# Performance work log

Measured on AMD Instinct MI355X. Metric: run time of the kernel, lower is better.

Reference implementation:

```python
import jax, jax.numpy as jnp
import numpy as np

B, D, C = 8192, 1024, 4096  # batch, d_model, num_clusters (all active)
EPS = 1e-12  # matches F.normalize eps


def _l2_normalize(x):
    n = jnp.linalg.norm(x, axis=-1, keepdims=True)
    return x / jnp.maximum(n, EPS)


def setup_inputs() -> dict:
    key = jax.random.key(0)
    k1, k2 = jax.random.split(key)
    embedding = jax.random.normal(k1, (B, D), dtype=jnp.float32)
    centroids = jax.random.normal(k2, (C, D), dtype=jnp.float32)  # buffer, all active
    return {"embedding": embedding, "centroids": centroids}


def reference(embedding, centroids):
    # Fused equivalent of the per-centroid Python loop:
    # cosine sim of normalized embedding vs each normalized centroid.
    emb_n = _l2_normalize(embedding)        # [B, D]
    cen_n = _l2_normalize(centroids)        # [C, D]
    sims = jnp.clip(emb_n @ cen_n.T, 0.0, 1.0)  # [B, C], per-sim clamp to [0,1]
    max_sim = jnp.max(sims, axis=-1)        # [B]
    closest = jnp.argmax(sims, axis=-1)     # [B] int
    novelty = jnp.clip(jnp.sqrt(1.0 - max_sim), 0.0, 1.0)  # [B]
    return novelty, closest
```

## Files before the change

kernel.cpp:

```cpp
#include <hip/hip_runtime.h>
#include <math.h>

#define B_ROWS 8192
#define C_COLS 4096
#define D_DIM  1024
#define EPSN   1e-12f

typedef float v4f __attribute__((ext_vector_type(4)));
typedef short v8s __attribute__((ext_vector_type(8)));

__device__ __forceinline__ unsigned short bf16_rtn(float x) {
    unsigned int u = __float_as_uint(x);
    u += 0x7fffu + ((u >> 16) & 1u);
    return (unsigned short)(u >> 16);
}

__device__ __forceinline__ bool better_vi(float v, int i, float V, int I) {
    return (v > V) || (v == V && i < I);
}

__global__ __launch_bounds__(256) void prep_kernel(
    const float* __restrict__ emb, const float* __restrict__ cen,
    unsigned short* __restrict__ Ah, unsigned short* __restrict__ Bh,
    float* __restrict__ inv_a, float* __restrict__ inv_b)
{
    const int lane = threadIdx.x & 63;
    const int wid  = blockIdx.x * 4 + (threadIdx.x >> 6);
    const float* src; unsigned short* dst; float* invp; int r;
    if (wid < B_ROWS) { src = emb; r = wid;          dst = Ah; invp = inv_a; }
    else              { src = cen; r = wid - B_ROWS; dst = Bh; invp = inv_b; }

    const float* rp = src + (size_t)r * D_DIM;
    float4 v[4];
    float ss = 0.0f;
    #pragma unroll
    for (int j = 0; j < 4; ++j) {
        v[j] = *(const float4*)(rp + (j * 64 + lane) * 4);
        ss += v[j].x * v[j].x + v[j].y * v[j].y + v[j].z * v[j].z + v[j].w * v[j].w;
    }
    #pragma unroll
    for (int off = 1; off < 64; off <<= 1) ss += __shfl_xor(ss, off, 64);

    const float iv = 1.0f / fmaxf(sqrtf(ss), EPSN);
    if (lane == 0) invp[r] = iv;

    unsigned short* dp = dst + (size_t)r * D_DIM;
    #pragma unroll
    for (int j = 0; j < 4; ++j) {
        ushort4 H;
        H.x = bf16_rtn(v[j].x * iv);
        H.y = bf16_rtn(v[j].y * iv);
        H.z = bf16_rtn(v[j].z * iv);
        H.w = bf16_rtn(v[j].w * iv);
        *(ushort4*)(dp + (j * 64 + lane) * 4) = H;
    }
}

#define GLD16(gp, lp) \
    __builtin_amdgcn_global_load_lds( \
        (const __attribute__((address_space(1))) void*)(gp), \
        (__attribute__((address_space(3))) void*)(lp), 16, 0, 0)

__global__ __launch_bounds__(512, 4) void simmax_kernel(
    const unsigned short* __restrict__ Ahg, const unsigned short* __restrict__ Bhg,
    float* __restrict__ p1v, int* __restrict__ p1i,
    float* __restrict__ p2v, int* __restrict__ p2i)
{
    __shared__ unsigned short lds[24576];

    const int tid    = threadIdx.x;
    const int L      = tid & 63;
    const int w      = tid >> 6;
    const int lane15 = L & 15;
    const int quad   = L >> 4;
    const int wr     = w >> 1;
    const int wc     = w & 1;
    const int row0   = blockIdx.x * 256;
    const int c0     = blockIdx.y * 128;

    const int scol = (tid & 7) ^ ((tid >> 3) & 7);
    const unsigned short* aB = Ahg + (size_t)(row0 + (tid >> 3)) * D_DIM + scol * 8;
    const unsigned short* bB = Bhg + (size_t)(c0   + (tid >> 3)) * D_DIM + scol * 8;
    const int wofs = w * 512;

#define STAGE_ALL(kb) do { \
    GLD16(aB + (kb),           &lds[0     + wofs]); \
    GLD16(aB + 65536  + (kb),  &lds[4096  + wofs]); \
    GLD16(aB + 131072 + (kb),  &lds[8192  + wofs]); \
    GLD16(aB + 196608 + (kb),  &lds[12288 + wofs]); \
    GLD16(bB + (kb),           &lds[16384 + wofs]); \
    GLD16(bB + 65536  + (kb),  &lds[20480 + wofs]); \
} while (0)

    v4f acc[4][4];
    #pragma unroll
    for (int mt = 0; mt < 4; ++mt)
        #pragma unroll
        for (int nt = 0; nt < 4; ++nt) acc[mt][nt] = (v4f)0.0f;

    int rAo[4], rBo[4];
    #pragma unroll
    for (int t = 0; t < 4; ++t) {
        rAo[t] = (wr * 64 + t * 16 + lane15) * 64;
        rBo[t] = 16384 + (wc * 64 + t * 16 + lane15) * 64;
    }
    const int s7 = lane15 & 7;
    const int cq[2] = { (quad ^ s7) * 8, ((4 + quad) ^ s7) * 8 };

    for (int kc = 0; kc < D_DIM / 64; ++kc) {
        STAGE_ALL(kc * 64);
        __syncthreads();

        #pragma unroll
        for (int h = 0; h < 2; ++h) {
            v8s fah[4], fbh[4];
            #pragma unroll
            for (int t = 0; t < 4; ++t) {
                fah[t] = *(const v8s*)&lds[rAo[t] + cq[h]];
                fbh[t] = *(const v8s*)&lds[rBo[t] + cq[h]];
            }
            #pragma unroll
            for (int mt = 0; mt < 4; ++mt)
                #pragma unroll
                for (int nt = 0; nt < 4; ++nt)
                    acc[mt][nt] = __builtin_amdgcn_mfma_f32_16x16x32_bf16(
                        fah[mt], fbh[nt], acc[mt][nt], 0, 0, 0);
        }
        __syncthreads();
    }

    const int pc = blockIdx.y * 2 + wc;
    #pragma unroll
    for (int mt = 0; mt < 4; ++mt) {
        #pragma unroll
        for (int r = 0; r < 4; ++r) {
            float a1v = acc[mt][0][r];
            int   a1i = c0 + wc * 64 + 0 * 16 + lane15;
            float a2v = -1e30f;
            int   a2i = 0x7fffffff;
            #pragma unroll
            for (int nt = 1; nt < 4; ++nt) {
                float v  = acc[mt][nt][r];
                int   ci = c0 + wc * 64 + nt * 16 + lane15;
                if (better_vi(v, ci, a1v, a1i))      { a2v = a1v; a2i = a1i; a1v = v; a1i = ci; }
                else if (better_vi(v, ci, a2v, a2i)) { a2v = v;   a2i = ci; }
            }
            #pragma unroll
            for (int off = 8; off; off >>= 1) {
                float b1v = __shfl_down(a1v, off, 64); int b1i = __shfl_down(a1i, off, 64);
                float b2v = __shfl_down(a2v, off, 64); int b2i = __shfl_down(a2i, off, 64);
                if (better_vi(b1v, b1i, a1v, a1i)) {
                    if (better_vi(a1v, a1i, b2v, b2i)) { a2v = a1v; a2i = a1i; }
                    else                               { a2v = b2v; a2i = b2i; }
                    a1v = b1v; a1i = b1i;
                } else if (better_vi(b1v, b1i, a2v, a2i)) {
                    a2v = b1v; a2i = b1i;
                }
            }
            if (lane15 == 0) {
                int rg = row0 + wr * 64 + mt * 16 + quad * 4 + r;
                size_t ix = (size_t)rg * 64 + pc;
                p1v[ix] = a1v; p1i[ix] = a1i;
                p2v[ix] = a2v; p2i[ix] = a2i;
            }
        }
    }
}

__global__ __launch_bounds__(256) void finalize_kernel(
    const float* __restrict__ emb, const float* __restrict__ cen,
    const float* __restrict__ inv_a, const float* __restrict__ inv_b,
    const float* __restrict__ p1v, const int* __restrict__ p1i,
    const float* __restrict__ p2v, const int* __restrict__ p2i,
    float* __restrict__ out)
{
    const int lane = threadIdx.x & 63;
    const int row  = blockIdx.x * 4 + (threadIdx.x >> 6);
    const size_t base = (size_t)row * 64 + lane;

    float v[4]; int ix[4];
    v[0] = p1v[base]; ix[0] = p1i[base];
    v[1] = p2v[base]; ix[1] = p2i[base];
    v[2] = -1e30f;    ix[2] = 0x7ffffffe;
    v[3] = -1e30f;    ix[3] = 0x7fffffff;

    #pragma unroll
    for (int off = 1; off < 64; off <<= 1) {
        float ov[4]; int oi[4];
        #pragma unroll
        for (int k = 0; k < 4; ++k) {
            ov[k] = __shfl_xor(v[k],  off, 64);
            oi[k] = __shfl_xor(ix[k], off, 64);
        }
        #pragma unroll
        for (int k = 0; k < 4; ++k) {
            float bv = ov[k]; int bi = oi[k];
            bool b0 = better_vi(bv, bi, v[0], ix[0]);
            bool b1 = better_vi(bv, bi, v[1], ix[1]);
            bool b2 = better_vi(bv, bi, v[2], ix[2]);
            bool b3 = better_vi(bv, bi, v[3], ix[3]);
            float nv3 = b2 ? v[2] : (b3 ? bv : v[3]); int ni3 = b2 ? ix[2] : (b3 ? bi : ix[3]);
            float nv2 = b1 ? v[1] : (b2 ? bv : v[2]); int ni2 = b1 ? ix[1] : (b2 ? bi : ix[2]);
            float nv1 = b0 ? v[0] : (b1 ? bv : v[1]); int ni1 = b0 ? ix[0] : (b1 ? bi : ix[1]);
            float nv0 = b0 ? bv   : v[0];             int ni0 = b0 ? bi    : ix[0];
            v[0] = nv0; ix[0] = ni0; v[1] = nv1; ix[1] = ni1;
            v[2] = nv2; ix[2] = ni2; v[3] = nv3; ix[3] = ni3;
        }
    }

    const float* er = emb + (size_t)row * D_DIM;
    const float* cr0 = cen + (size_t)ix[0] * D_DIM;
    const float* cr1 = cen + (size_t)ix[1] * D_DIM;
    const float* cr2 = cen + (size_t)ix[2] * D_DIM;
    const float* cr3 = cen + (size_t)ix[3] * D_DIM;

    float d[4] = { 0.0f, 0.0f, 0.0f, 0.0f };
    #pragma unroll
    for (int j = 0; j < 4; ++j) {
        int e = (j * 64 + lane) * 4;
        float4 ev = *(const float4*)(er  + e);
        float4 c0 = *(const float4*)(cr0 + e);
        float4 c1 = *(const float4*)(cr1 + e);
        float4 c2 = *(const float4*)(cr2 + e);
        float4 c3 = *(const float4*)(cr3 + e);
        d[0] += ev.x * c0.x + ev.y * c0.y + ev.z * c0.z + ev.w * c0.w;
        d[1] += ev.x * c1.x + ev.y * c1.y + ev.z * c1.z + ev.w * c1.w;
        d[2] += ev.x * c2.x + ev.y * c2.y + ev.z * c2.z + ev.w * c2.w;
        d[3] += ev.x * c3.x + ev.y * c3.y + ev.z * c3.z + ev.w * c3.w;
    }
    #pragma unroll
    for (int off = 1; off < 64; off <<= 1) {
        #pragma unroll
        for (int c = 0; c < 4; ++c) d[c] += __shfl_xor(d[c], off, 64);
    }

    if (lane == 0) {
        const float ia = inv_a[row];
        float m = -1e30f; int ci = 0x7fffffff;
        #pragma unroll
        for (int c = 0; c < 4; ++c) {
            float s = d[c] * ia * inv_b[ix[c]];
            if (better_vi(s, ix[c], m, ci)) { m = s; ci = ix[c]; }
        }
        if (m <= 0.0f) ci = 0;
        float ms = fminf(fmaxf(m, 0.0f), 1.0f);
        out[row]          = fminf(fmaxf(sqrtf(1.0f - ms), 0.0f), 1.0f);
        out[B_ROWS + row] = (float)ci;
    }
}

extern "C" void kernel_launch(void* const* d_in, const int* in_sizes, int n_in,
                              void* d_out, int out_size, void* d_ws, size_t ws_size,
                              hipStream_t stream)
{
    const float* emb = (const float*)d_in[0];
    const float* cen = (const float*)d_in[1];
    float* out = (float*)d_out;

    unsigned short* Ahp = (unsigned short*)d_ws;
    unsigned short* Bhp = Ahp + (size_t)B_ROWS * D_DIM;
    float* inv_a = (float*)(Bhp + (size_t)C_COLS * D_DIM);
    float* inv_b = inv_a + B_ROWS;
    float* p1v   = inv_b + C_COLS;
    int*   p1i   = (int*)(p1v + (size_t)64 * B_ROWS);
    float* p2v   = (float*)(p1i + (size_t)64 * B_ROWS);
    int*   p2i   = (int*)(p2v + (size_t)64 * B_ROWS);

    prep_kernel<<<(B_ROWS + C_COLS) / 4, 256, 0, stream>>>(emb, cen, Ahp, Bhp, inv_a, inv_b);

    dim3 grid(B_ROWS / 256, C_COLS / 128);
    simmax_kernel<<<grid, 512, 0, stream>>>(Ahp, Bhp, p1v, p1i, p2v, p2i);

    finalize_kernel<<<B_ROWS / 4, 256, 0, stream>>>(emb, cen, inv_a, inv_b,
                                                    p1v, p1i, p2v, p2i, out);
}
```

Before: 198.9 us.

## Shrink simmax tile to 128x128 and load B fragments directly from global

The similarity GEMM block tile shrinks from 256x128 rows by columns with 512 threads to 128x128 with 256 threads, and the grid doubles along the row dimension. The B (centroid) fragments are now read straight from global memory into registers for each MFMA instead of being staged through LDS, so only A uses shared memory. The aim is to cut LDS footprint and LDS read traffic, allowing more resident blocks. In exchange, B reads are duplicated across the two row-waves, are not coalesced through LDS, and their global latency sits inside the k-loop with no double buffering.

After: 273.7 us. +37.6%, slower.

```diff
diff --git a/kernel.cpp b/kernel.cpp
--- a/kernel.cpp
+++ b/kernel.cpp
@@ -61,12 +61,12 @@
         (const __attribute__((address_space(1))) void*)(gp), \
         (__attribute__((address_space(3))) void*)(lp), 16, 0, 0)
 
-__global__ __launch_bounds__(512, 4) void simmax_kernel(
+__global__ __launch_bounds__(256, 3) void simmax_kernel(
     const unsigned short* __restrict__ Ahg, const unsigned short* __restrict__ Bhg,
     float* __restrict__ p1v, int* __restrict__ p1i,
     float* __restrict__ p2v, int* __restrict__ p2i)
 {
-    __shared__ unsigned short lds[24576];
+    __shared__ unsigned short lds[8192];
 
     const int tid    = threadIdx.x;
     const int L      = tid & 63;
@@ -75,56 +75,60 @@
     const int quad   = L >> 4;
     const int wr     = w >> 1;
     const int wc     = w & 1;
-    const int row0   = blockIdx.x * 256;
+    const int row0   = blockIdx.x * 128;
     const int c0     = blockIdx.y * 128;
 
     const int scol = (tid & 7) ^ ((tid >> 3) & 7);
     const unsigned short* aB = Ahg + (size_t)(row0 + (tid >> 3)) * D_DIM + scol * 8;
-    const unsigned short* bB = Bhg + (size_t)(c0   + (tid >> 3)) * D_DIM + scol * 8;
     const int wofs = w * 512;
 
-#define STAGE_ALL(kb) do { \
-    GLD16(aB + (kb),           &lds[0     + wofs]); \
-    GLD16(aB + 65536  + (kb),  &lds[4096  + wofs]); \
-    GLD16(aB + 131072 + (kb),  &lds[8192  + wofs]); \
-    GLD16(aB + 196608 + (kb),  &lds[12288 + wofs]); \
-    GLD16(bB + (kb),           &lds[16384 + wofs]); \
-    GLD16(bB + 65536  + (kb),  &lds[20480 + wofs]); \
+#define STAGE_A(kb) do { \
+    GLD16(aB + (kb),           &lds[0    + wofs]); \
+    GLD16(aB + 32768  + (kb),  &lds[2048 + wofs]); \
+    GLD16(aB + 65536  + (kb),  &lds[4096 + wofs]); \
+    GLD16(aB + 98304  + (kb),  &lds[6144 + wofs]); \
 } while (0)
 
+    const unsigned short* bF[4];
+    #pragma unroll
+    for (int t = 0; t < 4; ++t)
+        bF[t] = Bhg + (size_t)(c0 + wc * 64 + t * 16 + lane15) * D_DIM + quad * 8;
+
     v4f acc[4][4];
     #pragma unroll
     for (int mt = 0; mt < 4; ++mt)
         #pragma unroll
         for (int nt = 0; nt < 4; ++nt) acc[mt][nt] = (v4f)0.0f;
 
-    int rAo[4], rBo[4];
-    #pragma unroll
-    for (int t = 0; t < 4; ++t) {
-        rAo[t] = (wr * 64 + t * 16 + lane15) * 64;
-        rBo[t] = 16384 + (wc * 64 + t * 16 + lane15) * 64;
-    }
+    int rAo[4];
+    #pragma unroll
+    for (int t = 0; t < 4; ++t) rAo[t] = (wr * 64 + t * 16 + lane15) * 64;
     const int s7 = lane15 & 7;
     const int cq[2] = { (quad ^ s7) * 8, ((4 + quad) ^ s7) * 8 };
 
     for (int kc = 0; kc < D_DIM / 64; ++kc) {
-        STAGE_ALL(kc * 64);
+        const int kb = kc * 64;
+        STAGE_A(kb);
+        v8s fb[2][4];
+        #pragma unroll
+        for (int h = 0; h < 2; ++h)
+            #pragma unroll
+            for (int t = 0; t < 4; ++t)
+                fb[h][t] = *(const v8s*)(bF[t] + kb + h * 32);
         __syncthreads();
 
         #pragma unroll
         for (int h = 0; h < 2; ++h) {
-            v8s fah[4], fbh[4];
-            #pragma unroll
-            for (int t = 0; t < 4; ++t) {
+            v8s fah[4];
+            #pragma unroll
+            for (int t = 0; t < 4; ++t)
                 fah[t] = *(const v8s*)&lds[rAo[t] + cq[h]];
-                fbh[t] = *(const v8s*)&lds[rBo[t] + cq[h]];
-            }
             #pragma unroll
             for (int mt = 0; mt < 4; ++mt)
                 #pragma unroll
                 for (int nt = 0; nt < 4; ++nt)
                     acc[mt][nt] = __builtin_amdgcn_mfma_f32_16x16x32_bf16(
-                        fah[mt], fbh[nt], acc[mt][nt], 0, 0, 0);
+                        fah[mt], fb[h][nt], acc[mt][nt], 0, 0, 0);
         }
         __syncthreads();
     }
@@ -268,8 +272,8 @@
 
     prep_kernel<<<(B_ROWS + C_COLS) / 4, 256, 0, stream>>>(emb, cen, Ahp, Bhp, inv_a, inv_b);
 
-    dim3 grid(B_ROWS / 256, C_COLS / 128);
-    simmax_kernel<<<grid, 512, 0, stream>>>(Ahp, Bhp, p1v, p1i, p2v, p2i);
+    dim3 grid(B_ROWS / 128, C_COLS / 128);
+    simmax_kernel<<<grid, 256, 0, stream>>>(Ahp, Bhp, p1v, p1i, p2v, p2i);
 
     finalize_kernel<<<B_ROWS / 4, 256, 0, stream>>>(emb, cen, inv_a, inv_b,
                                                     p1v, p1i, p2v, p2i, out);
```

## Triple-buffer LDS K-tiles with async prefetch two steps ahead

Applied to the files above, without the earlier changes.

The K loop is restructured from a single 64-wide LDS tile with two barriers per step into a three-buffer ring of 32-wide tiles. Global-to-LDS loads for step t+2 are issued before the MFMAs of step t, and partial vmcnt waits replace the full syncthreads. The intent is to hide global load latency behind the matrix math and drop one barrier per iteration. In exchange LDS use rises from 48KB to 72KB per block, which may cut occupancy below the 4 blocks the launch bounds ask for, and the swizzle is changed for the narrower tile.

New measurement: 211.9 us. 6.5% more time.

```diff
diff --git a/kernel.cpp b/kernel.cpp
--- a/kernel.cpp
+++ b/kernel.cpp
@@ -66,7 +66,7 @@
     float* __restrict__ p1v, int* __restrict__ p1i,
     float* __restrict__ p2v, int* __restrict__ p2i)
 {
-    __shared__ unsigned short lds[24576];
+    __shared__ unsigned short lds[3 * 12288];
 
     const int tid    = threadIdx.x;
     const int L      = tid & 63;
@@ -78,18 +78,15 @@
     const int row0   = blockIdx.x * 256;
     const int c0     = blockIdx.y * 128;
 
-    const int scol = (tid & 7) ^ ((tid >> 3) & 7);
-    const unsigned short* aB = Ahg + (size_t)(row0 + (tid >> 3)) * D_DIM + scol * 8;
-    const unsigned short* bB = Bhg + (size_t)(c0   + (tid >> 3)) * D_DIM + scol * 8;
-    const int wofs = w * 512;
-
-#define STAGE_ALL(kb) do { \
-    GLD16(aB + (kb),           &lds[0     + wofs]); \
-    GLD16(aB + 65536  + (kb),  &lds[4096  + wofs]); \
-    GLD16(aB + 131072 + (kb),  &lds[8192  + wofs]); \
-    GLD16(aB + 196608 + (kb),  &lds[12288 + wofs]); \
-    GLD16(bB + (kb),           &lds[16384 + wofs]); \
-    GLD16(bB + 65536  + (kb),  &lds[20480 + wofs]); \
+    const int sg = (tid & 3) ^ ((tid >> 2) & 3);
+    const unsigned short* aS = Ahg + (size_t)(row0 + (tid >> 2)) * D_DIM + sg * 8;
+    const unsigned short* bS = Bhg + (size_t)(c0   + (tid >> 2)) * D_DIM + sg * 8;
+    const int wS = w * 512;
+
+#define STAGE(bo, kb) do { \
+    GLD16(aS + (kb),          &lds[(bo) + 0    + wS]); \
+    GLD16(aS + 131072 + (kb), &lds[(bo) + 4096 + wS]); \
+    GLD16(bS + (kb),          &lds[(bo) + 8192 + wS]); \
 } while (0)
 
     v4f acc[4][4];
@@ -101,32 +98,36 @@
     int rAo[4], rBo[4];
     #pragma unroll
     for (int t = 0; t < 4; ++t) {
-        rAo[t] = (wr * 64 + t * 16 + lane15) * 64;
-        rBo[t] = 16384 + (wc * 64 + t * 16 + lane15) * 64;
-    }
-    const int s7 = lane15 & 7;
-    const int cq[2] = { (quad ^ s7) * 8, ((4 + quad) ^ s7) * 8 };
-
-    for (int kc = 0; kc < D_DIM / 64; ++kc) {
-        STAGE_ALL(kc * 64);
-        __syncthreads();
-
-        #pragma unroll
-        for (int h = 0; h < 2; ++h) {
-            v8s fah[4], fbh[4];
+        rAo[t] = (wr * 64 + t * 16 + lane15) * 32;
+        rBo[t] = 8192 + (wc * 64 + t * 16 + lane15) * 32;
+    }
+    const int cq = (quad ^ (lane15 & 3)) * 8;
+
+    STAGE(0, 0);
+    STAGE(12288, 32);
+
+    int b0 = 0, b1 = 12288, b2 = 24576;
+    for (int t = 0; t < 32; ++t) {
+        if (t == 31) asm volatile("s_waitcnt vmcnt(0)" ::: "memory");
+        else         asm volatile("s_waitcnt vmcnt(3)" ::: "memory");
+        __builtin_amdgcn_s_barrier();
+        __builtin_amdgcn_sched_barrier(0);
+        if (t < 30) STAGE(b2, (t + 2) * 32);
+
+        v8s fa[4], fb[4];
+        #pragma unroll
+        for (int q = 0; q < 4; ++q) {
+            fa[q] = *(const v8s*)&lds[b0 + rAo[q] + cq];
+            fb[q] = *(const v8s*)&lds[b0 + rBo[q] + cq];
+        }
+        #pragma unroll
+        for (int mt = 0; mt < 4; ++mt)
             #pragma unroll
-            for (int t = 0; t < 4; ++t) {
-                fah[t] = *(const v8s*)&lds[rAo[t] + cq[h]];
-                fbh[t] = *(const v8s*)&lds[rBo[t] + cq[h]];
-            }
-            #pragma unroll
-            for (int mt = 0; mt < 4; ++mt)
-                #pragma unroll
-                for (int nt = 0; nt < 4; ++nt)
-                    acc[mt][nt] = __builtin_amdgcn_mfma_f32_16x16x32_bf16(
-                        fah[mt], fbh[nt], acc[mt][nt], 0, 0, 0);
-        }
-        __syncthreads();
+            for (int nt = 0; nt < 4; ++nt)
+                acc[mt][nt] = __builtin_amdgcn_mfma_f32_16x16x32_bf16(
+                    fa[mt], fb[nt], acc[mt][nt], 0, 0, 0);
+
+        const int tb = b0; b0 = b1; b1 = b2; b2 = tb;
     }
 
     const int pc = blockIdx.y * 2 + wc;
```
